# Kernel optimization log

Measured on AMD Instinct MI355X. Metric: run time of the kernel, lower is better.

Reference implementation:

```python
import jax, jax.numpy as jnp
import numpy as np

N, M_CODES, Z_DIM = 4096, 4096, 1024


def setup_inputs() -> dict:
    key = jax.random.key(0)
    k1, k2 = jax.random.split(key)
    z = jax.random.normal(k1, (N, Z_DIM), dtype=jnp.float32)
    e = jax.random.normal(k2, (M_CODES, Z_DIM), dtype=jnp.float32)
    return {"z": z, "e": e}


def reference(z, e):
    # Squared pairwise L2 distances [N, M] via GEMM expansion:
    # ||z_i - e_j||^2 = ||z_i||^2 + ||e_j||^2 - 2 z_i . e_j
    z_sq = jnp.sum(z * z, axis=1)               # [N]
    e_sq = jnp.sum(e * e, axis=1)               # [M]
    cross = jnp.einsum('nd,md->nm', z, e)       # [N, M]
    dist = z_sq[:, None] + e_sq[None, :] - 2.0 * cross  # [N, M]
    # min over dim 0 (over data points N) -> per-code nearest distance [M]
    loss = jnp.mean(jnp.min(dist, axis=0))
    return loss
```

## Files before the change

### kernel.cpp

```cpp
#include <hip/hip_runtime.h>
#include <hip/hip_bf16.h>
#include <stdint.h>

#define N_PTS   4096
#define M_CODES 4096
#define ZDIM    1024

typedef __attribute__((ext_vector_type(4))) float f32x4;

__device__ __forceinline__ unsigned enc_f32(float f) {
    unsigned u = __float_as_uint(f);
    return (u & 0x80000000u) ? ~u : (u | 0x80000000u);
}
__device__ __forceinline__ float dec_f32(unsigned e) {
    unsigned u = (e & 0x80000000u) ? (e ^ 0x80000000u) : ~u;
    return __uint_as_float(u);
}

#define PREP_PITCH_B 1040
__global__ __launch_bounds__(256) void prep_kernel(
    const float* __restrict__ z, const float* __restrict__ e,
    uint8_t* __restrict__ zb, uint8_t* __restrict__ eb,
    float* __restrict__ zsq, float* __restrict__ esq,
    unsigned* __restrict__ min_enc) {
    __shared__ uint8_t tile[16 * PREP_PITCH_B];
    __shared__ float redbuf[16 * 4];

    const int t = threadIdx.x;
    const int b = blockIdx.x;
    if (b < 16) min_enc[b * 256 + t] = 0xFFFFFFFFu;

    const bool is_z = b < 256;
    const int rb = b & 255;
    const float* src = (is_z ? z : e) + (size_t)rb * 16 * ZDIM;
    uint8_t* dst = (is_z ? zb : eb) + (size_t)rb * 16384;
    const int w = t >> 6, lane = t & 63;

    #pragma unroll
    for (int it = 0; it < 16; it++) {
        float4 v = reinterpret_cast<const float4*>(src + (size_t)it * ZDIM)[t];
        int pk = 0;
        pk = __builtin_amdgcn_cvt_pk_fp8_f32(v.x, v.y, pk, false);
        pk = __builtin_amdgcn_cvt_pk_fp8_f32(v.z, v.w, pk, true);
        *reinterpret_cast<int*>(&tile[it * PREP_PITCH_B + t * 4]) = pk;
        float s = v.x * v.x + v.y * v.y + v.z * v.z + v.w * v.w;
        #pragma unroll
        for (int off = 1; off < 64; off <<= 1) s += __shfl_xor(s, off, 64);
        if (lane == 0) redbuf[it * 4 + w] = s;
    }
    __syncthreads();

    #pragma unroll
    for (int it2 = 0; it2 < 8; it2++) {
        const int c = it2 * 256 + t;
        const int kg = c >> 4, r16 = c & 15;
        const unsigned long long val = *reinterpret_cast<const unsigned long long*>(
            &tile[r16 * PREP_PITCH_B + kg * 8]);
        *reinterpret_cast<unsigned long long*>(&dst[(size_t)c * 8]) = val;
    }
    if (t < 16) {
        float sq = redbuf[t * 4] + redbuf[t * 4 + 1] +
                   redbuf[t * 4 + 2] + redbuf[t * 4 + 3];
        const int row = rb * 16 + t;
        if (is_z) zsq[row] = sq; else esq[row] = sq;
    }
}

__global__ __launch_bounds__(256, 4) void gemm_min_kernel(
    const uint8_t* __restrict__ zb, const uint8_t* __restrict__ eb,
    const float* __restrict__ zsq, unsigned* __restrict__ min_enc) {
    __shared__ __align__(16) uint8_t As[32768];
    __shared__ float zsq_s[128];
    __shared__ float colmin[2][128];

    const int t = threadIdx.x;
    const int bx = blockIdx.x;
    const int by = blockIdx.y;
    const int lane = t & 63;
    const int w = t >> 6;
    const int wm = w >> 1, wn = w & 1;
    const int lrow = lane & 15;
    const int q = lane >> 4;

    if (t < 128) zsq_s[t] = zsq[by * 128 + t];

    f32x4 acc[4][4];
    #pragma unroll
    for (int i = 0; i < 4; i++)
        #pragma unroll
        for (int j = 0; j < 4; j++) acc[i][j] = (f32x4){0.f, 0.f, 0.f, 0.f};

    const int seg_half = t >> 7;
    const int inner = (t & 127) * 16;
    const size_t a_seg0 = (size_t)(by * 8) * 16384;

    const uint8_t* b_base =
        eb + (size_t)(bx * 8 + wn * 4) * 16384 + lane * 8;

#define DMA_STAGE(st_)                                                        \
    {                                                                         \
        const int buf_ = ((st_) & 1) * 16384;                                 \
        const int koff_ = (st_) * 2048;           \
        _Pragma("unroll")                                                     \
        for (int j = 0; j < 4; j++) {                                         \
            const uint8_t* ga = zb + a_seg0 +                                 \
                (size_t)(j * 2 + seg_half) * 16384 + koff_ + inner;           \
            __builtin_amdgcn_global_load_lds(                                 \
                (const __attribute__((address_space(1))) void*)ga,            \
                (__attribute__((address_space(3))) void*)(As + buf_ +         \
                    (j * 2 + seg_half) * 2048 + inner), 16, 0, 0);            \
        }                                                                     \
    }

    DMA_STAGE(0);
    for (int st = 0; st < 8; st++) {
        __syncthreads();
        if (st < 7) DMA_STAGE(st + 1);
        const int buf = (st & 1) * 16384;
        const int koff = st * 2048;
        #pragma unroll
        for (int sl = 0; sl < 4; sl++) {
            long a[4], bb[4];
            #pragma unroll
            for (int an = 0; an < 4; an++)
                bb[an] = *(const long*)(b_base + (size_t)an * 16384 +
                                        koff + sl * 512);
            #pragma unroll
            for (int am = 0; am < 4; am++)
                a[am] = *(const long*)(As + buf + (wm * 4 + am) * 2048 +
                                       sl * 512 + lane * 8);
            #pragma unroll
            for (int am = 0; am < 4; am++)
                #pragma unroll
                for (int an = 0; an < 4; an++)
                    acc[am][an] = __builtin_amdgcn_mfma_f32_16x16x32_fp8_fp8(
                        a[am], bb[an], acc[am][an], 0, 0, 0);
        }
    }
#undef DMA_STAGE

    __syncthreads();

    #pragma unroll
    for (int an = 0; an < 4; an++) {
        float v = 3.4e38f;
        #pragma unroll
        for (int am = 0; am < 4; am++) {
            const int rbase = wm * 64 + am * 16 + q * 4;
            f32x4 c = acc[am][an];
            v = fminf(v, zsq_s[rbase + 0] - 2.f * c[0]);
            v = fminf(v, zsq_s[rbase + 1] - 2.f * c[1]);
            v = fminf(v, zsq_s[rbase + 2] - 2.f * c[2]);
            v = fminf(v, zsq_s[rbase + 3] - 2.f * c[3]);
        }
        v = fminf(v, __shfl_xor(v, 16, 64));
        v = fminf(v, __shfl_xor(v, 32, 64));
        if (q == 0) colmin[wm][wn * 64 + an * 16 + lrow] = v;
    }
    __syncthreads();
    if (t < 128) {
        const float m = fminf(colmin[0][t], colmin[1][t]);
        atomicMin(&min_enc[bx * 128 + t], enc_f32(m));
    }
}

__global__ __launch_bounds__(256) void finalize_kernel(
    const unsigned* __restrict__ min_enc, const float* __restrict__ esq,
    float* __restrict__ out) {
    const int t = threadIdx.x;
    float s = 0.f;
    #pragma unroll
    for (int i = 0; i < M_CODES / 256; i++) {
        const int j = i * 256 + t;
        s += dec_f32(min_enc[j]) + esq[j];
    }
    #pragma unroll
    for (int off = 1; off < 64; off <<= 1) s += __shfl_xor(s, off, 64);
    __shared__ float red[4];
    if ((t & 63) == 0) red[t >> 6] = s;
    __syncthreads();
    if (t == 0) out[0] = (red[0] + red[1] + red[2] + red[3]) * (1.f / M_CODES);
}

extern "C" void kernel_launch(void* const* d_in, const int* in_sizes, int n_in,
                              void* d_out, int out_size, void* d_ws, size_t ws_size,
                              hipStream_t stream) {
    (void)in_sizes; (void)n_in; (void)out_size; (void)ws_size;
    const float* z = (const float*)d_in[0];
    const float* e = (const float*)d_in[1];
    char* ws = (char*)d_ws;
    uint8_t* zb = (uint8_t*)ws;
    uint8_t* eb = (uint8_t*)(ws + ((size_t)4 << 20));
    float* zsq = (float*)(ws + ((size_t)8 << 20));
    float* esq = (float*)(ws + ((size_t)8 << 20) + 16384);
    unsigned* min_enc = (unsigned*)(ws + ((size_t)8 << 20) + 32768);

    prep_kernel<<<dim3(512), dim3(256), 0, stream>>>(
        z, e, zb, eb, zsq, esq, min_enc);
    gemm_min_kernel<<<dim3(32, 32), dim3(256), 0, stream>>>(
        zb, eb, zsq, min_enc);
    finalize_kernel<<<dim3(1), dim3(256), 0, stream>>>(min_enc, esq, (float*)d_out);
}
```

Baseline: 113.2 us.

## Switch to 16x16x128 scaled FP8 MFMA with regathered fragment loads

Replaces the four 16x16x32 FP8 MFMAs per K-slice with a single gfx950 mfma_scale 16x16x128 f8f6f4 instruction that uses unit scales, cutting the MFMA instruction count by a factor of four. Operand fragments are regathered so each lane holds 32 bytes assembled from four 8-byte loads at a q/lrow-dependent offset, matching the wider K layout. It also fixes a typo in dec_f32 that used the wrong variable for the negative branch, which changes the result rather than speed. The risks are that the k-ordering mapping is wrong and that register pressure rises from holding all B fragments for a stage at once.

```diff
diff --git a/kernel.cpp b/kernel.cpp
--- a/kernel.cpp
+++ b/kernel.cpp
@@ -7,13 +7,14 @@
 #define ZDIM    1024
 
 typedef __attribute__((ext_vector_type(4))) float f32x4;
+typedef __attribute__((ext_vector_type(8))) int   i32x8;
 
 __device__ __forceinline__ unsigned enc_f32(float f) {
     unsigned u = __float_as_uint(f);
     return (u & 0x80000000u) ? ~u : (u | 0x80000000u);
 }
 __device__ __forceinline__ float dec_f32(unsigned e) {
-    unsigned u = (e & 0x80000000u) ? (e ^ 0x80000000u) : ~u;
+    unsigned u = (e & 0x80000000u) ? (e ^ 0x80000000u) : ~e;
     return __uint_as_float(u);
 }
 
@@ -94,8 +95,9 @@
     const int inner = (t & 127) * 16;
     const size_t a_seg0 = (size_t)(by * 8) * 16384;
 
-    const uint8_t* b_base =
-        eb + (size_t)(bx * 8 + wn * 4) * 16384 + lane * 8;
+    const int frag_off = q * 512 + lrow * 8;
+    const uint8_t* b_frag =
+        eb + (size_t)(bx * 8 + wn * 4) * 16384 + frag_off;
 
 #define DMA_STAGE(st_)                                                        \
     {                                                                         \
@@ -112,29 +114,36 @@
         }                                                                     \
     }
 
+    union Frag { long l[4]; i32x8 v; };
+
     DMA_STAGE(0);
     for (int st = 0; st < 8; st++) {
         __syncthreads();
         if (st < 7) DMA_STAGE(st + 1);
         const int buf = (st & 1) * 16384;
         const int koff = st * 2048;
-        #pragma unroll
-        for (int sl = 0; sl < 4; sl++) {
-            long a[4], bb[4];
+
+        Frag bf[4];
+        #pragma unroll
+        for (int an = 0; an < 4; an++)
+            #pragma unroll
+            for (int p = 0; p < 4; p++)
+                bf[an].l[p] = *(const long*)(b_frag + (size_t)an * 16384 +
+                                             koff + p * 128);
+
+        #pragma unroll
+        for (int am = 0; am < 4; am++) {
+            Frag af;
+            #pragma unroll
+            for (int p = 0; p < 4; p++)
+                af.l[p] = *(const long*)(As + buf + (wm * 4 + am) * 2048 +
+                                         frag_off + p * 128);
             #pragma unroll
             for (int an = 0; an < 4; an++)
-                bb[an] = *(const long*)(b_base + (size_t)an * 16384 +
-                                        koff + sl * 512);
-            #pragma unroll
-            for (int am = 0; am < 4; am++)
-                a[am] = *(const long*)(As + buf + (wm * 4 + am) * 2048 +
-                                       sl * 512 + lane * 8);
-            #pragma unroll
-            for (int am = 0; am < 4; am++)
-                #pragma unroll
-                for (int an = 0; an < 4; an++)
-                    acc[am][an] = __builtin_amdgcn_mfma_f32_16x16x32_fp8_fp8(
-                        a[am], bb[an], acc[am][an], 0, 0, 0);
+                acc[am][an] = __builtin_amdgcn_mfma_scale_f32_16x16x128_f8f6f4(
+                    af.v, bf[an].v, acc[am][an],
+                    0 , 0 ,
+                    0, 0x7F7F7F7F, 0, 0x7F7F7F7F);
         }
     }
 #undef DMA_STAGE
```

New measurement: 146.2 us. 1.29x slower.

## Triple-buffer A tiles with finer K stages and explicit vmcnt waits

Applied to the files above, without the earlier changes.

Replaces the double-buffered 2048-byte K stages with a three-deep ring of 1024-byte stages, prefetching two stages ahead. Synchronisation uses manual s_waitcnt vmcnt and s_barrier in place of __syncthreads. B fragments are loaded from global memory at the top of each stage, ahead of the DMA issue, so their latency overlaps with the async LDS copies. The loop is fully unrolled with sched_barriers to fix instruction order. It also fixes the dec_f32 bug that used an uninitialised variable. Risks are more barriers per K and correctness depending on the vmcnt counts, since the B loads are also counted by vmcnt.

```diff
diff --git a/kernel.cpp b/kernel.cpp
--- a/kernel.cpp
+++ b/kernel.cpp
@@ -13,7 +13,7 @@
     return (u & 0x80000000u) ? ~u : (u | 0x80000000u);
 }
 __device__ __forceinline__ float dec_f32(unsigned e) {
-    unsigned u = (e & 0x80000000u) ? (e ^ 0x80000000u) : ~u;
+    unsigned u = (e & 0x80000000u) ? (e ^ 0x80000000u) : ~e;
     return __uint_as_float(u);
 }
 
@@ -69,7 +69,7 @@
 __global__ __launch_bounds__(256, 4) void gemm_min_kernel(
     const uint8_t* __restrict__ zb, const uint8_t* __restrict__ eb,
     const float* __restrict__ zsq, unsigned* __restrict__ min_enc) {
-    __shared__ __align__(16) uint8_t As[32768];
+    __shared__ __align__(16) uint8_t As[3 * 8192];
     __shared__ float zsq_s[128];
     __shared__ float colmin[2][128];
 
@@ -90,51 +90,88 @@
         #pragma unroll
         for (int j = 0; j < 4; j++) acc[i][j] = (f32x4){0.f, 0.f, 0.f, 0.f};
 
-    const int seg_half = t >> 7;
-    const int inner = (t & 127) * 16;
     const size_t a_seg0 = (size_t)(by * 8) * 16384;
-
     const uint8_t* b_base =
         eb + (size_t)(bx * 8 + wn * 4) * 16384 + lane * 8;
 
 #define DMA_STAGE(st_)                                                        \
     {                                                                         \
-        const int buf_ = ((st_) & 1) * 16384;                                 \
-        const int koff_ = (st_) * 2048;           \
+        const int buf_ = ((st_) % 3) * 8192;                                  \
         _Pragma("unroll")                                                     \
-        for (int j = 0; j < 4; j++) {                                         \
-            const uint8_t* ga = zb + a_seg0 +                                 \
-                (size_t)(j * 2 + seg_half) * 16384 + koff_ + inner;           \
+        for (int j = 0; j < 2; j++) {                                         \
+            const int seg_ = j * 4 + w;                                       \
+            const uint8_t* ga = zb + a_seg0 + (size_t)seg_ * 16384 +          \
+                (st_) * 1024 + lane * 16;                                     \
             __builtin_amdgcn_global_load_lds(                                 \
                 (const __attribute__((address_space(1))) void*)ga,            \
                 (__attribute__((address_space(3))) void*)(As + buf_ +         \
-                    (j * 2 + seg_half) * 2048 + inner), 16, 0, 0);            \
+                    seg_ * 1024 + lane * 16), 16, 0, 0);                      \
         }                                                                     \
     }
 
     DMA_STAGE(0);
-    for (int st = 0; st < 8; st++) {
-        __syncthreads();
-        if (st < 7) DMA_STAGE(st + 1);
-        const int buf = (st & 1) * 16384;
-        const int koff = st * 2048;
-        #pragma unroll
-        for (int sl = 0; sl < 4; sl++) {
-            long a[4], bb[4];
-            #pragma unroll
-            for (int an = 0; an < 4; an++)
-                bb[an] = *(const long*)(b_base + (size_t)an * 16384 +
-                                        koff + sl * 512);
-            #pragma unroll
-            for (int am = 0; am < 4; am++)
-                a[am] = *(const long*)(As + buf + (wm * 4 + am) * 2048 +
-                                       sl * 512 + lane * 8);
-            #pragma unroll
-            for (int am = 0; am < 4; am++)
-                #pragma unroll
-                for (int an = 0; an < 4; an++)
-                    acc[am][an] = __builtin_amdgcn_mfma_f32_16x16x32_fp8_fp8(
-                        a[am], bb[an], acc[am][an], 0, 0, 0);
+    DMA_STAGE(1);
+    asm volatile("s_waitcnt vmcnt(2)" ::: "memory");
+    __builtin_amdgcn_s_barrier();
+
+    #pragma unroll
+    for (int st = 0; st < 16; st++) {
+        const int buf = (st % 3) * 8192;
+        const int koff = st * 1024;
+
+        long bb0_0 = *(const long*)(b_base + 0 * 16384 + koff);
+        long bb0_1 = *(const long*)(b_base + 1 * 16384 + koff);
+        long bb0_2 = *(const long*)(b_base + 2 * 16384 + koff);
+        long bb0_3 = *(const long*)(b_base + 3 * 16384 + koff);
+        long bb1_0 = *(const long*)(b_base + 0 * 16384 + koff + 512);
+        long bb1_1 = *(const long*)(b_base + 1 * 16384 + koff + 512);
+        long bb1_2 = *(const long*)(b_base + 2 * 16384 + koff + 512);
+        long bb1_3 = *(const long*)(b_base + 3 * 16384 + koff + 512);
+        __builtin_amdgcn_sched_barrier(0);
+
+        if (st < 14) DMA_STAGE(st + 2);
+
+        #pragma unroll
+        for (int sl = 0; sl < 2; sl++) {
+            long a0 = *(const long*)(As + buf + (wm * 4 + 0) * 1024 +
+                                     sl * 512 + lane * 8);
+            long a1 = *(const long*)(As + buf + (wm * 4 + 1) * 1024 +
+                                     sl * 512 + lane * 8);
+            long a2 = *(const long*)(As + buf + (wm * 4 + 2) * 1024 +
+                                     sl * 512 + lane * 8);
+            long a3 = *(const long*)(As + buf + (wm * 4 + 3) * 1024 +
+                                     sl * 512 + lane * 8);
+            const long b0 = sl ? bb1_0 : bb0_0;
+            const long b1 = sl ? bb1_1 : bb0_1;
+            const long b2 = sl ? bb1_2 : bb0_2;
+            const long b3 = sl ? bb1_3 : bb0_3;
+            acc[0][0] = __builtin_amdgcn_mfma_f32_16x16x32_fp8_fp8(a0, b0, acc[0][0], 0, 0, 0);
+            acc[0][1] = __builtin_amdgcn_mfma_f32_16x16x32_fp8_fp8(a0, b1, acc[0][1], 0, 0, 0);
+            acc[0][2] = __builtin_amdgcn_mfma_f32_16x16x32_fp8_fp8(a0, b2, acc[0][2], 0, 0, 0);
+            acc[0][3] = __builtin_amdgcn_mfma_f32_16x16x32_fp8_fp8(a0, b3, acc[0][3], 0, 0, 0);
+            acc[1][0] = __builtin_amdgcn_mfma_f32_16x16x32_fp8_fp8(a1, b0, acc[1][0], 0, 0, 0);
+            acc[1][1] = __builtin_amdgcn_mfma_f32_16x16x32_fp8_fp8(a1, b1, acc[1][1], 0, 0, 0);
+            acc[1][2] = __builtin_amdgcn_mfma_f32_16x16x32_fp8_fp8(a1, b2, acc[1][2], 0, 0, 0);
+            acc[1][3] = __builtin_amdgcn_mfma_f32_16x16x32_fp8_fp8(a1, b3, acc[1][3], 0, 0, 0);
+            acc[2][0] = __builtin_amdgcn_mfma_f32_16x16x32_fp8_fp8(a2, b0, acc[2][0], 0, 0, 0);
+            acc[2][1] = __builtin_amdgcn_mfma_f32_16x16x32_fp8_fp8(a2, b1, acc[2][1], 0, 0, 0);
+            acc[2][2] = __builtin_amdgcn_mfma_f32_16x16x32_fp8_fp8(a2, b2, acc[2][2], 0, 0, 0);
+            acc[2][3] = __builtin_amdgcn_mfma_f32_16x16x32_fp8_fp8(a2, b3, acc[2][3], 0, 0, 0);
+            acc[3][0] = __builtin_amdgcn_mfma_f32_16x16x32_fp8_fp8(a3, b0, acc[3][0], 0, 0, 0);
+            acc[3][1] = __builtin_amdgcn_mfma_f32_16x16x32_fp8_fp8(a3, b1, acc[3][1], 0, 0, 0);
+            acc[3][2] = __builtin_amdgcn_mfma_f32_16x16x32_fp8_fp8(a3, b2, acc[3][2], 0, 0, 0);
+            acc[3][3] = __builtin_amdgcn_mfma_f32_16x16x32_fp8_fp8(a3, b3, acc[3][3], 0, 0, 0);
+        }
+
+        if (st < 15) {
+            __builtin_amdgcn_sched_barrier(0);
+            if (st < 14) {
+                asm volatile("s_waitcnt vmcnt(2)" ::: "memory");
+            } else {
+                asm volatile("s_waitcnt vmcnt(0)" ::: "memory");
+            }
+            __builtin_amdgcn_s_barrier();
+            __builtin_amdgcn_sched_barrier(0);
         }
     }
 #undef DMA_STAGE
```

After: 106.8 us. -5.7%, faster.
